# Kernel optimization log

Measured on AMD Instinct MI355X. Metric: run time of the kernel, lower is better.

## Reference

```python
import jax, jax.numpy as jnp
import numpy as np

V, D, H, F, L, B, S = 32000, 1024, 16, 4096, 6, 2, 1024
DH = D // H


def setup_inputs() -> dict:
    key = jax.random.key(0)
    ks = jax.random.split(key, 12)
    n = lambda k, shape: jax.random.normal(k, shape, jnp.float32) * 0.02
    inp = {}
    inp['x'] = jax.random.randint(ks[0], (B, S), 0, V)
    # causal mask: 1 = masked (upper triangle), matches masked_fill(mask==1, -inf)
    inp['mask'] = jnp.triu(jnp.ones((S, S), jnp.int32), k=1)[None, None]
    inp['embed'] = n(ks[1], (V, D))
    inp['wq'] = n(ks[2], (L, D, D)); inp['bq'] = jnp.zeros((L, D), jnp.float32)
    inp['wk'] = n(ks[3], (L, D, D)); inp['bk'] = jnp.zeros((L, D), jnp.float32)
    inp['wv'] = n(ks[4], (L, D, D)); inp['bv'] = jnp.zeros((L, D), jnp.float32)
    inp['wo'] = n(ks[5], (L, D, D)); inp['bo'] = jnp.zeros((L, D), jnp.float32)
    inp['w1'] = n(ks[6], (L, D, F)); inp['b1'] = jnp.zeros((L, F), jnp.float32)
    inp['w2'] = n(ks[7], (L, F, D)); inp['b2'] = jnp.zeros((L, D), jnp.float32)
    inp['ln1_g'] = jnp.ones((L, D), jnp.float32); inp['ln1_b'] = jnp.zeros((L, D), jnp.float32)
    inp['ln2_g'] = jnp.ones((L, D), jnp.float32); inp['ln2_b'] = jnp.zeros((L, D), jnp.float32)
    inp['lnf_g'] = jnp.ones((D,), jnp.float32); inp['lnf_b'] = jnp.zeros((D,), jnp.float32)
    inp['proj_w'] = n(ks[8], (D, V)); inp['proj_b'] = jnp.zeros((V,), jnp.float32)
    return inp


def _layernorm(x, g, b, eps=1e-5):
    mu = jnp.mean(x, axis=-1, keepdims=True)
    var = jnp.var(x, axis=-1, keepdims=True)
    return (x - mu) * jax.lax.rsqrt(var + eps) * g + b


def _positional_encoding(s, d):
    pos = jnp.arange(s, dtype=jnp.float32)[:, None]
    div = jnp.exp(jnp.arange(0, d, 2, dtype=jnp.float32) * (-jnp.log(10000.0) / d))
    pe = jnp.zeros((s, d), jnp.float32)
    pe = pe.at[:, 0::2].set(jnp.sin(pos * div))
    pe = pe.at[:, 1::2].set(jnp.cos(pos * div))
    return pe


def reference(x, mask, embed, wq, bq, wk, bk, wv, bv, wo, bo, w1, b1, w2, b2,
              ln1_g, ln1_b, ln2_g, ln2_b, lnf_g, lnf_b, proj_w, proj_b):
    b_, s_ = x.shape
    h = embed[x] * jnp.sqrt(jnp.float32(D))          # [B,S,D]
    h = h + _positional_encoding(s_, D)[None]
    scale = 1.0 / jnp.sqrt(jnp.float32(DH))

    def layer(h, p):
        Wq, Bq, Wk, Bk, Wv, Bv, Wo, Bo, W1, B1, W2, B2, G1, Be1, G2, Be2 = p
        q = (h @ Wq + Bq).reshape(b_, s_, H, DH).transpose(0, 2, 1, 3)   # [B,H,S,Dh]
        k = (h @ Wk + Bk).reshape(b_, s_, H, DH).transpose(0, 2, 1, 3)
        v = (h @ Wv + Bv).reshape(b_, s_, H, DH).transpose(0, 2, 1, 3)
        scores = jnp.einsum('bhqd,bhkd->bhqk', q, k) * scale            # [B,H,S,S]
        scores = jnp.where(mask == 1, -jnp.inf, scores)
        attn = jax.nn.softmax(scores, axis=-1)
        ctx = jnp.einsum('bhqk,bhkd->bhqd', attn, v)
        ctx = ctx.transpose(0, 2, 1, 3).reshape(b_, s_, D) @ Wo + Bo
        h = _layernorm(h + ctx, G1, Be1)
        ffn = jax.nn.relu(h @ W1 + B1) @ W2 + B2
        h = _layernorm(h + ffn, G2, Be2)
        return h, None

    h, _ = jax.lax.scan(layer, h, (wq, bq, wk, bk, wv, bv, wo, bo,
                                   w1, b1, w2, b2, ln1_g, ln1_b, ln2_g, ln2_b))
    h = _layernorm(h, lnf_g, lnf_b)
    return h @ proj_w + proj_b                                           # [B,S,V]
```

## Files before the change

### kernel.cpp

```cpp
#include <hip/hip_runtime.h>
#include <math.h>

#define D_MODEL 1024
#define NHEADS 16
#define DHEAD 64
#define FDIM 4096
#define NLAYERS 6
#define BATCH 2
#define SEQ 1024
#define NROWS (BATCH*SEQ)
#define VOCAB 32000

typedef __attribute__((ext_vector_type(4))) float f32x4;
typedef __attribute__((ext_vector_type(4))) __bf16 bf16x4;
typedef __attribute__((ext_vector_type(8))) __bf16 bf16x8;

__device__ __forceinline__ void gll16(const void* g, void* l) {
  __builtin_amdgcn_global_load_lds(
      (const __attribute__((address_space(1))) unsigned int*)g,
      (__attribute__((address_space(3))) unsigned int*)l, 16, 0, 0);
}

__global__ __launch_bounds__(256) void transpose_w(
    const float* __restrict__ W, __bf16* __restrict__ Wt, int K, int N,
    size_t out_lstride, int row_off) {
  __shared__ __bf16 Ls[64][68];
  const float* Wl = W + (size_t)blockIdx.z * K * N;
  __bf16* Wtl = Wt + (size_t)blockIdx.z * out_lstride + (size_t)row_off * K;
  const int n0 = blockIdx.x * 64, k0 = blockIdx.y * 64;
  const int tid = threadIdx.x;
  #pragma unroll
  for (int p = 0; p < 4; ++p) {
    int e = tid + p * 256;
    int r = e >> 4, c4 = (e & 15) * 4;
    float4 v = *(const float4*)&Wl[(size_t)(k0 + r) * N + n0 + c4];
    Ls[c4 + 0][r] = (__bf16)v.x; Ls[c4 + 1][r] = (__bf16)v.y;
    Ls[c4 + 2][r] = (__bf16)v.z; Ls[c4 + 3][r] = (__bf16)v.w;
  }
  __syncthreads();
  #pragma unroll
  for (int p = 0; p < 4; ++p) {
    int e = tid + p * 256;
    int r2 = e >> 4, c8 = (e & 15) * 4;
    bf16x4 o{Ls[r2][c8], Ls[r2][c8 + 1], Ls[r2][c8 + 2], Ls[r2][c8 + 3]};
    *(bf16x4*)&Wtl[(size_t)(n0 + r2) * K + k0 + c8] = o;
  }
}

struct GemmP {
  const __bf16* A;
  const __bf16* W[3];
  const float* B[3];
  void* C[3];
  int N, K;
};

template<int BM, int RELU, int OUTF32, int MULTIBIAS>
__global__ __launch_bounds__(256) void gemm_bf16(GemmP g) {
  constexpr int BK = 64;
  const __bf16* __restrict__ A = g.A;
  const __bf16* __restrict__ W = g.W[blockIdx.z];
  const int N = g.N, K = g.K;

  __shared__ __bf16 As[2][BM * BK];
  __shared__ __bf16 Bs[2][128 * BK];

  const int tid = threadIdx.x;
  const int lane = tid & 63, w = tid >> 6;

  const int gx = gridDim.x;
  const int nblk = gx * gridDim.y;
  const int id = blockIdx.x + blockIdx.y * gx;
  const int per = nblk >> 3;
  const int sid = (id & 7) * per + (id >> 3);
  const int row0 = (sid % gx) * BM;
  const int col0 = (sid / gx) * 128;

  const int wm = w >> 1, wn = w & 1;
  const int lr = lane & 15, rsw = lr & 7;

  constexpr int MI = BM / 32;
  f32x4 acc[MI][4] = {};

  const int swg = ((lane & 7) ^ (lane >> 3)) * 8;
  const __bf16* Ag = A + (size_t)(row0 + w * (BM / 4) + (lane >> 3)) * K + swg;
  const __bf16* Wg = W + (size_t)(col0 + w * 32 + (lane >> 3)) * K + swg;

  const int NT = K / BK;

  auto stage = [&](int buf, int t) {
    const int k0 = t * BK;
    #pragma unroll
    for (int s = 0; s < BM / 32; ++s)
      gll16(Ag + (size_t)s * 8 * K + k0, &As[buf][(w * (BM / 4) + s * 8) * BK]);
    #pragma unroll
    for (int s = 0; s < 4; ++s)
      gll16(Wg + (size_t)s * 8 * K + k0, &Bs[buf][(w * 32 + s * 8) * BK]);
  };

  stage(0, 0);
  __syncthreads();

  int cur = 0;
  for (int t = 0; t < NT; ++t) {
    if (t + 1 < NT) stage(cur ^ 1, t + 1);
    #pragma unroll
    for (int kk = 0; kk < 2; ++kk) {
      const int gsw = ((kk * 4 + (lane >> 4)) ^ rsw) * 8;
      bf16x8 af[MI], bf[4];
      #pragma unroll
      for (int i = 0; i < MI; ++i)
        af[i] = *(const bf16x8*)&As[cur][(wm * (BM / 2) + i * 16 + lr) * BK + gsw];
      #pragma unroll
      for (int j = 0; j < 4; ++j)
        bf[j] = *(const bf16x8*)&Bs[cur][(wn * 64 + j * 16 + lr) * BK + gsw];
      #pragma unroll
      for (int i = 0; i < MI; ++i)
        #pragma unroll
        for (int j = 0; j < 4; ++j)
          acc[i][j] = __builtin_amdgcn_mfma_f32_16x16x32_bf16(af[i], bf[j], acc[i][j], 0, 0, 0);
    }
    __syncthreads();
    cur ^= 1;
  }

  #pragma unroll
  for (int i = 0; i < MI; ++i) {
    #pragma unroll
    for (int j = 0; j < 4; ++j) {
      int col = col0 + wn * 64 + j * 16 + lr;
      float bb = MULTIBIAS ? g.B[col >> 10][col & 1023] : g.B[blockIdx.z][col];
      #pragma unroll
      for (int r = 0; r < 4; ++r) {
        int row = row0 + wm * (BM / 2) + i * 16 + (lane >> 4) * 4 + r;
        float v = acc[i][j][r] + bb;
        if (RELU) v = fmaxf(v, 0.0f);
        if (OUTF32) ((float*)g.C[blockIdx.z])[(size_t)row * N + col] = v;
        else ((__bf16*)g.C[blockIdx.z])[(size_t)row * N + col] = (__bf16)v;
      }
    }
  }
}

__global__ __launch_bounds__(512, 2) void gemm_256(
    const __bf16* __restrict__ A, const __bf16* __restrict__ W,
    const float* __restrict__ bias, float* __restrict__ C, int N, int K) {
  extern __shared__ __bf16 sm[];
  __bf16* Asm = sm;
  __bf16* Bsm = sm + 2 * 256 * 64;

  const int tid = threadIdx.x;
  const int lane = tid & 63, w = tid >> 6;

  const int gx = gridDim.x;
  const int nblk = gx * gridDim.y;
  const int id = blockIdx.x + blockIdx.y * gx;
  const int per = nblk >> 3;
  const int sid = (id & 7) * per + (id >> 3);
  const int row0 = (sid % gx) * 256;
  const int col0 = (sid / gx) * 256;

  const int wr = w >> 2, wc = w & 3;
  const int lr = lane & 15;

  f32x4 acc[8][4] = {};

  const int swg = ((lane & 7) ^ (lane >> 3)) * 8;
  const __bf16* Agb = A + (size_t)(row0 + (lane >> 3)) * K + swg;
  const __bf16* Wgb = W + (size_t)(col0 + (lane >> 3)) * K + swg;

  const int NT = K / 64;

  auto stage_half = [&](int idx) {
    const int tile = idx >> 2, half = idx & 3;
    const int buf = tile & 1;
    const int k0 = tile * 64;
    const int rowbase = (half & 1) * 128 + w * 16;
    const __bf16* src = (half < 2 ? Wgb : Agb) + (size_t)rowbase * K + k0;
    __bf16* dst = (half < 2 ? Bsm : Asm) + buf * 16384 + rowbase * 64;
    gll16(src, dst);
    gll16(src + (size_t)8 * K, dst + 8 * 64);
  };

  #pragma unroll
  for (int i = 0; i < 5; ++i) stage_half(i);
  asm volatile("s_waitcnt vmcnt(2)" ::: "memory");
  __builtin_amdgcn_s_barrier();

  for (int t = 0; t < NT; ++t) {
    const int cur = t & 1;
    bf16x8 bfr[4][2];
    #pragma unroll
    for (int h = 0; h < 4; ++h) {
      if (h == 0) {
        #pragma unroll
        for (int j = 0; j < 4; ++j) {
          int row = wc * 64 + j * 16 + lr;
          #pragma unroll
          for (int kk = 0; kk < 2; ++kk)
            bfr[j][kk] = *(const bf16x8*)&Bsm[cur * 16384 + row * 64 +
                                              (((kk * 4 + (lane >> 4)) ^ (row & 7)) * 8)];
        }
      }
      bf16x8 afr[2][2];
      #pragma unroll
      for (int ii = 0; ii < 2; ++ii) {
        int row = wr * 128 + (2 * h + ii) * 16 + lr;
        #pragma unroll
        for (int kk = 0; kk < 2; ++kk)
          afr[ii][kk] = *(const bf16x8*)&Asm[cur * 16384 + row * 64 +
                                             (((kk * 4 + (lane >> 4)) ^ (row & 7)) * 8)];
      }
      const int sidx = 4 * t + h + 5;
      if (sidx < 4 * NT) stage_half(sidx);
      if (h == 3) {
        if (t + 2 < NT) asm volatile("s_waitcnt vmcnt(2)" ::: "memory");
        else if (t + 1 < NT) asm volatile("s_waitcnt vmcnt(0)" ::: "memory");
      }
      __builtin_amdgcn_s_barrier();
      __builtin_amdgcn_s_setprio(1);
      #pragma unroll
      for (int kk = 0; kk < 2; ++kk)
        #pragma unroll
        for (int ii = 0; ii < 2; ++ii)
          #pragma unroll
          for (int j = 0; j < 4; ++j)
            acc[2 * h + ii][j] = __builtin_amdgcn_mfma_f32_16x16x32_bf16(
                afr[ii][kk], bfr[j][kk], acc[2 * h + ii][j], 0, 0, 0);
      __builtin_amdgcn_s_setprio(0);
      __builtin_amdgcn_s_barrier();
    }
  }

  #pragma unroll
  for (int i = 0; i < 8; ++i) {
    #pragma unroll
    for (int j = 0; j < 4; ++j) {
      int col = col0 + wc * 64 + j * 16 + lr;
      float bb = bias[col];
      #pragma unroll
      for (int r = 0; r < 4; ++r) {
        int row = row0 + wr * 128 + i * 16 + (lane >> 4) * 4 + r;
        C[(size_t)row * N + col] = acc[i][j][r] + bb;
      }
    }
  }
}

__global__ __launch_bounds__(512) void attn_kernel(
    const __bf16* __restrict__ QKV, __bf16* __restrict__ O) {
  __shared__ __bf16 Ks[64 * 64];
  __shared__ __bf16 Vts[64 * 64];
  __shared__ __bf16 Psm[8][16 * 64];

  const int tid = threadIdx.x;
  const int lane = tid & 63, w = tid >> 6;
  const int q0 = blockIdx.x * 128;
  const int bh = blockIdx.y;
  const int b = bh >> 4, h = bh & 15;
  const size_t qb = ((size_t)b * SEQ) * 3072 + (size_t)h * DHEAD;
  const size_t ob = ((size_t)b * SEQ) * D_MODEL + (size_t)h * DHEAD;

  const int lr = lane & 15;
  const int lk = (lane >> 4) * 8;

  bf16x8 qa[2];
  {
    const __bf16* qp = QKV + qb + (size_t)(q0 + w * 16 + lr) * 3072;
    qa[0] = *(const bf16x8*)&qp[lk];
    qa[1] = *(const bf16x8*)&qp[32 + lk];
  }

  f32x4 o_acc[4] = {};
  float m[4], l[4];
  #pragma unroll
  for (int r = 0; r < 4; ++r) { m[r] = -1e30f; l[r] = 0.0f; }

  const int nck = q0 / 64 + 2;

  for (int ck = 0; ck < nck; ++ck) {
    const int kv0 = ck * 64;
    __syncthreads();
    {
      int r = tid >> 3, d8 = (tid & 7) * 8;
      const size_t grow = qb + (size_t)(kv0 + r) * 3072 + d8;
      bf16x8 kv = *(const bf16x8*)&QKV[grow + 1024];
      *(bf16x8*)&Ks[(r * 64 + d8) ^ ((r & 7) << 3)] = kv;
      bf16x8 vv = *(const bf16x8*)&QKV[grow + 2048];
      #pragma unroll
      for (int j = 0; j < 8; ++j)
        Vts[((d8 + j) * 64 + r) ^ (((d8 + j) & 7) << 3)] = vv[j];
    }
    __syncthreads();

    f32x4 s_acc[4] = {};
    #pragma unroll
    for (int t = 0; t < 4; ++t) {
      int row = t * 16 + lr;
      #pragma unroll
      for (int hh = 0; hh < 2; ++hh) {
        bf16x8 kb = *(const bf16x8*)&Ks[(row * 64 + hh * 32 + lk) ^ ((row & 7) << 3)];
        s_acc[t] = __builtin_amdgcn_mfma_f32_16x16x32_bf16(qa[hh], kb, s_acc[t], 0, 0, 0);
      }
    }

    #pragma unroll
    for (int t = 0; t < 4; ++t) {
      int kvg = kv0 + t * 16 + lr;
      #pragma unroll
      for (int r = 0; r < 4; ++r) {
        float sv = s_acc[t][r] * 0.125f;
        int qg = q0 + w * 16 + (lane >> 4) * 4 + r;
        if (kvg > qg) sv = -1e30f;
        s_acc[t][r] = sv;
      }
    }

    #pragma unroll
    for (int r = 0; r < 4; ++r) {
      float cm = fmaxf(fmaxf(s_acc[0][r], s_acc[1][r]), fmaxf(s_acc[2][r], s_acc[3][r]));
      #pragma unroll
      for (int off = 1; off < 16; off <<= 1) cm = fmaxf(cm, __shfl_xor(cm, off, 64));
      float newm = fmaxf(m[r], cm);
      float sc = __expf(m[r] - newm);
      m[r] = newm;
      float psum = 0.0f;
      #pragma unroll
      for (int t = 0; t < 4; ++t) {
        float p = __expf(s_acc[t][r] - newm);
        s_acc[t][r] = p;
        psum += p;
      }
      #pragma unroll
      for (int off = 1; off < 16; off <<= 1) psum += __shfl_xor(psum, off, 64);
      l[r] = l[r] * sc + psum;
      #pragma unroll
      for (int t = 0; t < 4; ++t) o_acc[t][r] *= sc;
    }

    #pragma unroll
    for (int t = 0; t < 4; ++t) {
      #pragma unroll
      for (int r = 0; r < 4; ++r) {
        int ql = (lane >> 4) * 4 + r;
        Psm[w][(ql * 64 + t * 16 + lr) ^ ((ql & 7) << 3)] = (__bf16)(s_acc[t][r]);
      }
    }

    bf16x8 pa[2];
    #pragma unroll
    for (int hh = 0; hh < 2; ++hh)
      pa[hh] = *(const bf16x8*)&Psm[w][(lr * 64 + hh * 32 + lk) ^ ((lr & 7) << 3)];
    #pragma unroll
    for (int t = 0; t < 4; ++t) {
      int row = t * 16 + lr;
      #pragma unroll
      for (int hh = 0; hh < 2; ++hh) {
        bf16x8 vb = *(const bf16x8*)&Vts[(row * 64 + hh * 32 + lk) ^ ((row & 7) << 3)];
        o_acc[t] = __builtin_amdgcn_mfma_f32_16x16x32_bf16(pa[hh], vb, o_acc[t], 0, 0, 0);
      }
    }
  }

  #pragma unroll
  for (int r = 0; r < 4; ++r) {
    float inv = 1.0f / l[r];
    int qg = q0 + w * 16 + (lane >> 4) * 4 + r;
    #pragma unroll
    for (int t = 0; t < 4; ++t)
      O[ob + (size_t)qg * D_MODEL + t * 16 + lr] = (__bf16)(o_acc[t][r] * inv);
  }
}

template<int HASRES>
__global__ __launch_bounds__(256) void addln_kernel(
    const __bf16* __restrict__ X, const __bf16* __restrict__ Rr,
    const float* __restrict__ g, const float* __restrict__ bb,
    __bf16* __restrict__ Out) {
  const int row = blockIdx.x;
  const int tid = threadIdx.x;
  const size_t rb = (size_t)row * D_MODEL + tid * 4;
  bf16x4 xv = *(const bf16x4*)&X[rb];
  float v[4];
  float s = 0.0f, ss = 0.0f;
  if (HASRES) {
    bf16x4 rv = *(const bf16x4*)&Rr[rb];
    #pragma unroll
    for (int i = 0; i < 4; ++i) {
      v[i] = (float)xv[i] + (float)rv[i];
      s += v[i]; ss += v[i] * v[i];
    }
  } else {
    #pragma unroll
    for (int i = 0; i < 4; ++i) { v[i] = (float)xv[i]; s += v[i]; ss += v[i] * v[i]; }
  }
  #pragma unroll
  for (int off = 32; off; off >>= 1) { s += __shfl_xor(s, off, 64); ss += __shfl_xor(ss, off, 64); }
  __shared__ float red[8];
  const int lane = tid & 63, w = tid >> 6;
  if (lane == 0) { red[w] = s; red[4 + w] = ss; }
  __syncthreads();
  s = red[0] + red[1] + red[2] + red[3];
  ss = red[4] + red[5] + red[6] + red[7];
  float mean = s * (1.0f / D_MODEL);
  float var = ss * (1.0f / D_MODEL) - mean * mean;
  float rs = rsqrtf(var + 1e-5f);
  const int d0 = tid * 4;
  bf16x4 ov;
  #pragma unroll
  for (int i = 0; i < 4; ++i)
    ov[i] = (__bf16)((v[i] - mean) * rs * g[d0 + i] + bb[d0 + i]);
  *(bf16x4*)&Out[rb] = ov;
}

__global__ __launch_bounds__(256) void embed_kernel(
    const int* __restrict__ x, const float* __restrict__ embed,
    __bf16* __restrict__ H) {
  const int row = blockIdx.x;
  const int spos = row & (SEQ - 1);
  const int tok = x[row];
  const int tid = threadIdx.x;
  const int d0 = tid * 4;
  float4 e4 = *(const float4*)&embed[(size_t)tok * D_MODEL + d0];
  float ev[4] = {e4.x, e4.y, e4.z, e4.w};
  bf16x4 ov;
  #pragma unroll
  for (int i = 0; i < 4; ++i) {
    int d = d0 + i;
    float div = expf((float)(2 * (d >> 1)) * (-9.2103403719761836f / (float)D_MODEL));
    float ang = (float)spos * div;
    float pe = (d & 1) ? cosf(ang) : sinf(ang);
    ov[i] = (__bf16)(ev[i] * 32.0f + pe);
  }
  *(bf16x4*)&H[(size_t)row * D_MODEL + d0] = ov;
}

extern "C" void kernel_launch(void* const* d_in, const int* in_sizes, int n_in,
                              void* d_out, int out_size, void* d_ws, size_t ws_size,
                              hipStream_t stream) {
  const int* x = (const int*)d_in[0];
  const float* embed = (const float*)d_in[2];
  const float* wq = (const float*)d_in[3];
  const float* bq = (const float*)d_in[4];
  const float* wk = (const float*)d_in[5];
  const float* bk = (const float*)d_in[6];
  const float* wv = (const float*)d_in[7];
  const float* bv = (const float*)d_in[8];
  const float* wo = (const float*)d_in[9];
  const float* bo = (const float*)d_in[10];
  const float* w1 = (const float*)d_in[11];
  const float* b1 = (const float*)d_in[12];
  const float* w2 = (const float*)d_in[13];
  const float* b2 = (const float*)d_in[14];
  const float* ln1g = (const float*)d_in[15];
  const float* ln1b = (const float*)d_in[16];
  const float* ln2g = (const float*)d_in[17];
  const float* ln2b = (const float*)d_in[18];
  const float* lnfg = (const float*)d_in[19];
  const float* lnfb = (const float*)d_in[20];
  const float* pw = (const float*)d_in[21];
  const float* pb = (const float*)d_in[22];
  float* out = (float*)d_out;

  char* wsp = (char*)d_ws;
  size_t off = 0;
  auto alloc = [&](size_t bytes) {
    void* p = wsp + off; off = (off + bytes + 255) & ~(size_t)255; return p;
  };
  const size_t RD2 = (size_t)NROWS * D_MODEL * 2;
  __bf16* Xb   = (__bf16*)alloc(RD2);
  __bf16* QKVb = (__bf16*)alloc((size_t)NROWS * 3072 * 2);
  __bf16* CTXb = (__bf16*)alloc(RD2);
  __bf16* Tb   = (__bf16*)alloc(RD2);
  __bf16* H1b  = (__bf16*)alloc(RD2);
  __bf16* FFb  = QKVb;
  const size_t DD = (size_t)D_MODEL * D_MODEL;
  const size_t DF = (size_t)D_MODEL * FDIM;
  const size_t D3 = (size_t)3072 * D_MODEL;
  __bf16* wqkvt = (__bf16*)alloc(NLAYERS * D3 * 2);
  __bf16* wot = (__bf16*)alloc(NLAYERS * DD * 2);
  __bf16* w1t = (__bf16*)alloc(NLAYERS * DF * 2);
  __bf16* w2t = (__bf16*)alloc(NLAYERS * DF * 2);
  __bf16* pwt = (__bf16*)alloc((size_t)D_MODEL * VOCAB * 2);

  transpose_w<<<dim3(16, 16, NLAYERS), 256, 0, stream>>>(wq, wqkvt, D_MODEL, D_MODEL, D3, 0);
  transpose_w<<<dim3(16, 16, NLAYERS), 256, 0, stream>>>(wk, wqkvt, D_MODEL, D_MODEL, D3, 1024);
  transpose_w<<<dim3(16, 16, NLAYERS), 256, 0, stream>>>(wv, wqkvt, D_MODEL, D_MODEL, D3, 2048);
  transpose_w<<<dim3(16, 16, NLAYERS), 256, 0, stream>>>(wo, wot, D_MODEL, D_MODEL, DD, 0);
  transpose_w<<<dim3(64, 16, NLAYERS), 256, 0, stream>>>(w1, w1t, D_MODEL, FDIM, DF, 0);
  transpose_w<<<dim3(16, 64, NLAYERS), 256, 0, stream>>>(w2, w2t, FDIM, D_MODEL, DF, 0);
  transpose_w<<<dim3(500, 16, 1), 256, 0, stream>>>(pw, pwt, D_MODEL, VOCAB, (size_t)D_MODEL * VOCAB, 0);

  embed_kernel<<<NROWS, 256, 0, stream>>>(x, embed, Xb);

  for (int l = 0; l < NLAYERS; ++l) {
    GemmP g{};
    g.A = Xb; g.N = 3072; g.K = D_MODEL;
    g.W[0] = wqkvt + l * D3;
    g.B[0] = bq + l * D_MODEL; g.B[1] = bk + l * D_MODEL; g.B[2] = bv + l * D_MODEL;
    g.C[0] = QKVb;
    gemm_bf16<64, 0, 0, 1><<<dim3(NROWS / 64, 3072 / 128, 1), 256, 0, stream>>>(g);

    attn_kernel<<<dim3(SEQ / 128, BATCH * NHEADS), 512, 0, stream>>>(QKVb, CTXb);

    GemmP go{};
    go.A = CTXb; go.N = D_MODEL; go.K = D_MODEL;
    go.W[0] = wot + l * DD; go.B[0] = bo + l * D_MODEL; go.C[0] = Tb;
    gemm_bf16<64, 0, 0, 0><<<dim3(NROWS / 64, D_MODEL / 128, 1), 256, 0, stream>>>(go);

    addln_kernel<1><<<NROWS, 256, 0, stream>>>(Xb, Tb, ln1g + l * D_MODEL, ln1b + l * D_MODEL, H1b);

    GemmP g1{};
    g1.A = H1b; g1.N = FDIM; g1.K = D_MODEL;
    g1.W[0] = w1t + l * DF; g1.B[0] = b1 + l * FDIM; g1.C[0] = FFb;
    gemm_bf16<128, 1, 0, 0><<<dim3(NROWS / 128, FDIM / 128, 1), 256, 0, stream>>>(g1);

    GemmP g2{};
    g2.A = FFb; g2.N = D_MODEL; g2.K = FDIM;
    g2.W[0] = w2t + l * DF; g2.B[0] = b2 + l * D_MODEL; g2.C[0] = Tb;
    gemm_bf16<64, 0, 0, 0><<<dim3(NROWS / 64, D_MODEL / 128, 1), 256, 0, stream>>>(g2);

    addln_kernel<1><<<NROWS, 256, 0, stream>>>(H1b, Tb, ln2g + l * D_MODEL, ln2b + l * D_MODEL, Xb);
  }

  addln_kernel<0><<<NROWS, 256, 0, stream>>>(Xb, nullptr, lnfg, lnfb, H1b);

  hipFuncSetAttribute((const void*)gemm_256,
                      hipFuncAttributeMaxDynamicSharedMemorySize, 131072);
  gemm_256<<<dim3(NROWS / 256, VOCAB / 256), 512, 131072, stream>>>(
      H1b, pwt, pb, out, VOCAB, D_MODEL);
}
```

Before: 1.520 ms.

## Rewrite 256x256 GEMM as 4-stage K=32 pipeline and use it for QKV/FFN1

Replaces the double-buffered K=64 staging of the 256x256 GEMM with a four-buffer ring of K=32 tiles, using a new swizzle and one barrier per iteration. The kernel is templated over ReLU, output type and multi-bias so it can also serve the QKV projection and the first FFN GEMM, replacing the smaller 64/128-tile GEMMs there. The goal is deeper prefetch, fewer barriers and more reuse per tile on large GEMMs. In exchange, grids for QKV (96 blocks) and FFN1 (128 blocks) become small relative to the CU count, which may leave the device under-filled.

```diff
diff --git a/kernel.cpp b/kernel.cpp
--- a/kernel.cpp
+++ b/kernel.cpp
@@ -142,12 +142,9 @@
   }
 }
 
-__global__ __launch_bounds__(512, 2) void gemm_256(
-    const __bf16* __restrict__ A, const __bf16* __restrict__ W,
-    const float* __restrict__ bias, float* __restrict__ C, int N, int K) {
+template<int RELU, int OUTF32, int MULTIBIAS>
+__global__ __launch_bounds__(512, 2) void gemm_256d(GemmP g) {
   extern __shared__ __bf16 sm[];
-  __bf16* Asm = sm;
-  __bf16* Bsm = sm + 2 * 256 * 64;
 
   const int tid = threadIdx.x;
   const int lane = tid & 63, w = tid >> 6;
@@ -162,74 +159,56 @@
 
   const int wr = w >> 2, wc = w & 3;
   const int lr = lane & 15;
+  const int N = g.N, K = g.K;
 
   f32x4 acc[8][4] = {};
 
-  const int swg = ((lane & 7) ^ (lane >> 3)) * 8;
-  const __bf16* Agb = A + (size_t)(row0 + (lane >> 3)) * K + swg;
-  const __bf16* Wgb = W + (size_t)(col0 + (lane >> 3)) * K + swg;
-
-  const int NT = K / 64;
-
-  auto stage_half = [&](int idx) {
-    const int tile = idx >> 2, half = idx & 3;
-    const int buf = tile & 1;
-    const int k0 = tile * 64;
-    const int rowbase = (half & 1) * 128 + w * 16;
-    const __bf16* src = (half < 2 ? Wgb : Agb) + (size_t)rowbase * K + k0;
-    __bf16* dst = (half < 2 ? Bsm : Asm) + buf * 16384 + rowbase * 64;
-    gll16(src, dst);
-    gll16(src + (size_t)8 * K, dst + 8 * 64);
+  const int sg = ((lane & 3) ^ ((lane >> 3) & 3)) * 8;
+  const __bf16* Ag = g.A + (size_t)(row0 + w * 32 + (lane >> 2)) * K + sg;
+  const __bf16* Wg = g.W[0] + (size_t)(col0 + w * 32 + (lane >> 2)) * K + sg;
+
+  const int NT = K / 32;
+
+  auto stage = [&](int t) {
+    const int k0 = t * 32;
+    __bf16* As = sm + (t & 3) * 16384;
+    __bf16* Bs = As + 8192;
+    gll16(Ag + k0, As + (w * 32) * 32);
+    gll16(Ag + (size_t)16 * K + k0, As + (w * 32 + 16) * 32);
+    gll16(Wg + k0, Bs + (w * 32) * 32);
+    gll16(Wg + (size_t)16 * K + k0, Bs + (w * 32 + 16) * 32);
   };
 
-  #pragma unroll
-  for (int i = 0; i < 5; ++i) stage_half(i);
-  asm volatile("s_waitcnt vmcnt(2)" ::: "memory");
-  __builtin_amdgcn_s_barrier();
+  stage(0); stage(1); stage(2);
 
   for (int t = 0; t < NT; ++t) {
-    const int cur = t & 1;
-    bf16x8 bfr[4][2];
-    #pragma unroll
-    for (int h = 0; h < 4; ++h) {
-      if (h == 0) {
-        #pragma unroll
-        for (int j = 0; j < 4; ++j) {
-          int row = wc * 64 + j * 16 + lr;
-          #pragma unroll
-          for (int kk = 0; kk < 2; ++kk)
-            bfr[j][kk] = *(const bf16x8*)&Bsm[cur * 16384 + row * 64 +
-                                              (((kk * 4 + (lane >> 4)) ^ (row & 7)) * 8)];
-        }
-      }
-      bf16x8 afr[2][2];
-      #pragma unroll
-      for (int ii = 0; ii < 2; ++ii) {
-        int row = wr * 128 + (2 * h + ii) * 16 + lr;
-        #pragma unroll
-        for (int kk = 0; kk < 2; ++kk)
-          afr[ii][kk] = *(const bf16x8*)&Asm[cur * 16384 + row * 64 +
-                                             (((kk * 4 + (lane >> 4)) ^ (row & 7)) * 8)];
-      }
-      const int sidx = 4 * t + h + 5;
-      if (sidx < 4 * NT) stage_half(sidx);
-      if (h == 3) {
-        if (t + 2 < NT) asm volatile("s_waitcnt vmcnt(2)" ::: "memory");
-        else if (t + 1 < NT) asm volatile("s_waitcnt vmcnt(0)" ::: "memory");
-      }
-      __builtin_amdgcn_s_barrier();
-      __builtin_amdgcn_s_setprio(1);
-      #pragma unroll
-      for (int kk = 0; kk < 2; ++kk)
-        #pragma unroll
-        for (int ii = 0; ii < 2; ++ii)
-          #pragma unroll
-          for (int j = 0; j < 4; ++j)
-            acc[2 * h + ii][j] = __builtin_amdgcn_mfma_f32_16x16x32_bf16(
-                afr[ii][kk], bfr[j][kk], acc[2 * h + ii][j], 0, 0, 0);
-      __builtin_amdgcn_s_setprio(0);
-      __builtin_amdgcn_s_barrier();
-    }
+    if (t + 2 < NT) asm volatile("s_waitcnt vmcnt(8)" ::: "memory");
+    else if (t + 1 < NT) asm volatile("s_waitcnt vmcnt(4)" ::: "memory");
+    else asm volatile("s_waitcnt vmcnt(0)" ::: "memory");
+    __builtin_amdgcn_s_barrier();
+    __builtin_amdgcn_sched_barrier(0);
+
+    const __bf16* As = sm + (t & 3) * 16384;
+    const __bf16* Bs = As + 8192;
+    const int kg = lane >> 4;
+
+    bf16x8 bfr[4];
+    #pragma unroll
+    for (int j = 0; j < 4; ++j) {
+      int row = wc * 64 + j * 16 + lr;
+      bfr[j] = *(const bf16x8*)&Bs[row * 32 + ((kg ^ ((row >> 1) & 3)) << 3)];
+    }
+    if (t + 3 < NT) stage(t + 3);
+    __builtin_amdgcn_s_setprio(1);
+    #pragma unroll
+    for (int i = 0; i < 8; ++i) {
+      int row = wr * 128 + i * 16 + lr;
+      bf16x8 af = *(const bf16x8*)&As[row * 32 + ((kg ^ ((row >> 1) & 3)) << 3)];
+      #pragma unroll
+      for (int j = 0; j < 4; ++j)
+        acc[i][j] = __builtin_amdgcn_mfma_f32_16x16x32_bf16(af, bfr[j], acc[i][j], 0, 0, 0);
+    }
+    __builtin_amdgcn_s_setprio(0);
   }
 
   #pragma unroll
@@ -237,11 +216,14 @@
     #pragma unroll
     for (int j = 0; j < 4; ++j) {
       int col = col0 + wc * 64 + j * 16 + lr;
-      float bb = bias[col];
+      float bb = MULTIBIAS ? g.B[col >> 10][col & 1023] : g.B[0][col];
       #pragma unroll
       for (int r = 0; r < 4; ++r) {
         int row = row0 + wr * 128 + i * 16 + (lane >> 4) * 4 + r;
-        C[(size_t)row * N + col] = acc[i][j][r] + bb;
+        float v = acc[i][j][r] + bb;
+        if (RELU) v = fmaxf(v, 0.0f);
+        if (OUTF32) ((float*)g.C[0])[(size_t)row * N + col] = v;
+        else ((__bf16*)g.C[0])[(size_t)row * N + col] = (__bf16)v;
       }
     }
   }
@@ -493,13 +475,20 @@
 
   embed_kernel<<<NROWS, 256, 0, stream>>>(x, embed, Xb);
 
+  hipFuncSetAttribute((const void*)gemm_256d<0, 1, 0>,
+                      hipFuncAttributeMaxDynamicSharedMemorySize, 131072);
+  hipFuncSetAttribute((const void*)gemm_256d<1, 0, 0>,
+                      hipFuncAttributeMaxDynamicSharedMemorySize, 131072);
+  hipFuncSetAttribute((const void*)gemm_256d<0, 0, 1>,
+                      hipFuncAttributeMaxDynamicSharedMemorySize, 131072);
+
   for (int l = 0; l < NLAYERS; ++l) {
     GemmP g{};
     g.A = Xb; g.N = 3072; g.K = D_MODEL;
     g.W[0] = wqkvt + l * D3;
     g.B[0] = bq + l * D_MODEL; g.B[1] = bk + l * D_MODEL; g.B[2] = bv + l * D_MODEL;
     g.C[0] = QKVb;
-    gemm_bf16<64, 0, 0, 1><<<dim3(NROWS / 64, 3072 / 128, 1), 256, 0, stream>>>(g);
+    gemm_256d<0, 0, 1><<<dim3(NROWS / 256, 3072 / 256), 512, 131072, stream>>>(g);
 
     attn_kernel<<<dim3(SEQ / 128, BATCH * NHEADS), 512, 0, stream>>>(QKVb, CTXb);
 
@@ -513,7 +502,7 @@
     GemmP g1{};
     g1.A = H1b; g1.N = FDIM; g1.K = D_MODEL;
     g1.W[0] = w1t + l * DF; g1.B[0] = b1 + l * FDIM; g1.C[0] = FFb;
-    gemm_bf16<128, 1, 0, 0><<<dim3(NROWS / 128, FDIM / 128, 1), 256, 0, stream>>>(g1);
+    gemm_256d<1, 0, 0><<<dim3(NROWS / 256, FDIM / 256), 512, 131072, stream>>>(g1);
 
     GemmP g2{};
     g2.A = FFb; g2.N = D_MODEL; g2.K = FDIM;
@@ -525,8 +514,8 @@
 
   addln_kernel<0><<<NROWS, 256, 0, stream>>>(Xb, nullptr, lnfg, lnfb, H1b);
 
-  hipFuncSetAttribute((const void*)gemm_256,
-                      hipFuncAttributeMaxDynamicSharedMemorySize, 131072);
-  gemm_256<<<dim3(NROWS / 256, VOCAB / 256), 512, 131072, stream>>>(
-      H1b, pwt, pb, out, VOCAB, D_MODEL);
-}
+  GemmP gp{};
+  gp.A = H1b; gp.N = VOCAB; gp.K = D_MODEL;
+  gp.W[0] = pwt; gp.B[0] = pb; gp.C[0] = out;
+  gemm_256d<0, 1, 0><<<dim3(NROWS / 256, VOCAB / 256), 512, 131072, stream>>>(gp);
+}
```

Result: slower. 1.647 ms (+8.3%).
